# Kernel tuning notes

Hardware: AMD Instinct MI355X
Metric: run time of the kernel (lower is better)

Reference implementation:

```python
import jax, jax.numpy as jnp
import numpy as np

ALPHA = 0.2      # LeakyReLU slope
KNN_RANK = 6     # adj keeps ranks <= 6 (7 nearest incl. self)
NEG = -1e12


def _gat_layer(x, adj, W, a, concat):
    # x: [B,N,Cin], W: [Cin,Cout], a: [2*Cout,1]
    h = jnp.matmul(x, W)                      # [B,N,C]
    C = W.shape[1]
    f1 = jnp.matmul(h, a[:C, 0])              # [B,N]  a1^T h_i
    f2 = jnp.matmul(h, a[C:, 0])              # [B,N]  a2^T h_j
    e = jax.nn.leaky_relu(f1[:, :, None] + f2[:, None, :], ALPHA)  # [B,N,N]
    e = jnp.where(adj > 0, e, NEG)
    att = jax.nn.softmax(e, axis=2)
    hp = jnp.einsum('bij,bjc->bic', att, h)
    return jax.nn.relu(hp) if concat else hp


def _knn_adj(y):
    # y: [B,N,C]; euclidean cdist then rank-threshold (argsort.argsort <= 6)
    sq = jnp.sum(y * y, axis=-1)              # [B,N]
    d2 = sq[:, :, None] + sq[:, None, :] - 2.0 * jnp.einsum('bic,bjc->bij', y, y)
    dist = jnp.sqrt(jnp.clip(d2, 0.0))
    ranks = jnp.argsort(jnp.argsort(dist, axis=2), axis=2)
    return jax.lax.stop_gradient((ranks <= KNN_RANK).astype(y.dtype))


def reference(x, w_head, b_head, W0, a0, W1, a1, W_out, a_out, w_last, b_last):
    # head conv: k=3, stride=2, pad=1
    y = jax.lax.conv_general_dilated(
        x, w_head, window_strides=(2, 2), padding=((1, 1), (1, 1)),
        dimension_numbers=('NCHW', 'OIHW', 'NCHW')) + b_head[None, :, None, None]
    B, C, H, W = y.shape
    N = H * W
    yn = jnp.transpose(y.reshape(B, C, N), (0, 2, 1))   # [B,N,C]
    adj = _knn_adj(yn)

    # GAT: two concat heads, then out head, elu, log_softmax over channels
    h = jnp.concatenate([_gat_layer(yn, adj, W0, a0, True),
                         _gat_layer(yn, adj, W1, a1, True)], axis=2)
    out = jax.nn.elu(_gat_layer(h, adj, W_out, a_out, False))
    out = jax.nn.log_softmax(out, axis=2)               # [B,N,C]

    Ho = int(np.sqrt(N))
    z = jnp.transpose(out, (0, 2, 1)).reshape(B, C, Ho, Ho)
    # ConvTranspose2d(k=3, s=2, pad=1, output_pad=1) == dilated conv with
    # flipped, transposed kernel; padding low=k-1-p=1, high=k-1-p+op=2
    w_eq = jnp.flip(w_last, axis=(2, 3)).swapaxes(0, 1)  # (out,in,kh,kw)
    z = jax.lax.conv_general_dilated(
        z, w_eq, window_strides=(1, 1), padding=((1, 2), (1, 2)),
        lhs_dilation=(2, 2), dimension_numbers=('NCHW', 'OIHW', 'NCHW'))
    return z + b_last[None, :, None, None]


def setup_inputs() -> dict:
    key = jax.random.key(0)
    ks = jax.random.split(key, 12)
    Cin, Cout = 31, 64
    s = 0.05
    return {
        'x': jax.random.normal(ks[0], (2, Cin, 128, 128), jnp.float32),
        'w_head': jax.random.normal(ks[1], (Cout, Cin, 3, 3), jnp.float32) * s,
        'b_head': jnp.zeros((Cout,), jnp.float32),
        'W0': jax.random.normal(ks[2], (Cout, Cout), jnp.float32) * s,
        'a0': jax.random.normal(ks[3], (2 * Cout, 1), jnp.float32) * s,
        'W1': jax.random.normal(ks[4], (Cout, Cout), jnp.float32) * s,
        'a1': jax.random.normal(ks[5], (2 * Cout, 1), jnp.float32) * s,
        'W_out': jax.random.normal(ks[6], (2 * Cout, Cout), jnp.float32) * s,
        'a_out': jax.random.normal(ks[7], (2 * Cout, 1), jnp.float32) * s,
        'w_last': jax.random.normal(ks[8], (Cout, Cout, 3, 3), jnp.float32) * s,  # torch (in,out,kh,kw)
        'b_last': jnp.zeros((Cout,), jnp.float32),
    }
```

## Files before the change

### kernel.cpp

```cpp
#include <hip/hip_runtime.h>
#include <math.h>

#define B2     2
#define CIN    31
#define CC     64
#define NN     4096
#define NCH    8

typedef short bf16x8 __attribute__((ext_vector_type(8)));
typedef float f32x4  __attribute__((ext_vector_type(4)));

__device__ inline unsigned short f2bf(float f) {
  union { float f; unsigned u; } v; v.f = f;
  unsigned r = (v.u + 0x7fffu + ((v.u >> 16) & 1u)) >> 16;
  return (unsigned short)r;
}
__device__ inline float bf2f(unsigned short h) {
  union { float f; unsigned u; } v; v.u = ((unsigned)h) << 16;
  return v.f;
}

constexpr int OF_YN   = 0;
constexpr int OF_SQ   = OF_YN   + B2*NN*CC;
constexpr int OF_HCAT = OF_SQ   + B2*NN;
constexpr int OF_FV   = OF_HCAT + B2*NN*128;
constexpr int OF_HAGG = OF_FV   + 4*B2*NN;
constexpr int OF_HO   = OF_HAGG + B2*NN*128;
constexpr int OF_FO   = OF_HO   + B2*NN*CC;
constexpr int OF_Z    = OF_FO   + 2*B2*NN;
constexpr int OF_PD   = OF_Z    + B2*NN*CC;
constexpr int OF_PI   = OF_PD   + B2*NN*NCH*7;
constexpr int OF_NBR  = OF_PI   + B2*NN*NCH*7;
constexpr int OF_WT   = OF_NBR  + B2*NN*7;
constexpr int OF_WHT  = OF_WT   + 9*64*64;
constexpr int OF_YNH  = OF_WHT  + 279*64;
constexpr int OF_YNL  = OF_YNH  + B2*NN*CC/2;

__global__ __launch_bounds__(256) void k_prep(const float* __restrict__ wlast,
                                              const float* __restrict__ whead,
                                              float* __restrict__ wT,
                                              float* __restrict__ whT) {
  int idx = blockIdx.x*256 + threadIdx.x;
  if (idx < 36864) {
    int co = idx & 63, ci = (idx >> 6) & 63, kk = idx >> 12;
    wT[idx] = wlast[(ci*64 + co)*9 + kk];
  } else if (idx < 36864 + 279*64) {
    int j = idx - 36864;
    int c = j & 63, q = j >> 6;
    whT[j] = whead[c*279 + q];
  }
}

__global__ __launch_bounds__(256) void k_head(const float* __restrict__ x,
                                              const float* __restrict__ whT,
                                              const float* __restrict__ bias,
                                              float* __restrict__ yn,
                                              float* __restrict__ sq,
                                              unsigned short* __restrict__ ynh,
                                              unsigned short* __restrict__ ynl) {
  int lane = threadIdx.x & 63, wv = threadIdx.x >> 6;
  int gbase = blockIdx.x*8 + wv*2;
  __shared__ __align__(16) float patch[4][2][280];
  for (int nn = 0; nn < 2; ++nn) {
    int g = gbase + nn;
    int b = g >> 12, n = g & 4095;
    int oh = n >> 6, ow = n & 63;
    for (int q = lane; q < 279; q += 64) {
      int ci = q / 9, r = q - ci*9;
      int ky = r / 3, kx = r - ky*3;
      int ih = 2*oh - 1 + ky, iw = 2*ow - 1 + kx;
      float v = 0.f;
      if (ih >= 0 && ih < 128 && iw >= 0 && iw < 128)
        v = x[((b*CIN + ci)*128 + ih)*128 + iw];
      patch[wv][nn][q] = v;
    }
  }
  __syncthreads();
  int c = lane;
  float acc[2];
  float bv = bias[c];
  acc[0] = bv; acc[1] = bv;
  for (int q = 0; q < 276; q += 4) {
    float w0 = whT[q*64 + c];
    float w1 = whT[(q+1)*64 + c];
    float w2 = whT[(q+2)*64 + c];
    float w3 = whT[(q+3)*64 + c];
    #pragma unroll
    for (int nn = 0; nn < 2; ++nn) {
      float4 pv = *(const float4*)&patch[wv][nn][q];
      acc[nn] = fmaf(pv.x, w0, acc[nn]);
      acc[nn] = fmaf(pv.y, w1, acc[nn]);
      acc[nn] = fmaf(pv.z, w2, acc[nn]);
      acc[nn] = fmaf(pv.w, w3, acc[nn]);
    }
  }
  for (int q = 276; q < 279; ++q) {
    float wq = whT[q*64 + c];
    #pragma unroll
    for (int nn = 0; nn < 2; ++nn) acc[nn] = fmaf(patch[wv][nn][q], wq, acc[nn]);
  }
  for (int nn = 0; nn < 2; ++nn) {
    int g = gbase + nn;
    float y = acc[nn];
    yn[g*64 + c] = y;
    unsigned short hb = f2bf(y);
    ynh[g*64 + c] = hb;
    ynl[g*64 + c] = f2bf(y - bf2f(hb));
    float s = y*y;
    #pragma unroll
    for (int off = 32; off > 0; off >>= 1) s += __shfl_xor(s, off);
    if (lane == 0) sq[g] = s;
  }
}

__global__ __launch_bounds__(256, 4) void k_knn6(const unsigned short* __restrict__ ynh,
                                                 const unsigned short* __restrict__ ynl,
                                                 const float* __restrict__ sq,
                                                 float* __restrict__ pd,
                                                 int* __restrict__ pidx) {
  __shared__ __align__(16) unsigned short Bh[2][64*72];
  __shared__ __align__(16) unsigned short Bl[2][64*72];
  __shared__ __align__(16) float sqjs[2][64];

  int b = blockIdx.z, ib = blockIdx.x, jsp = blockIdx.y;
  int i0 = ib*64, jbase = jsp*512;
  int tid = threadIdx.x;
  int lane = tid & 63, w = tid >> 6;
  int quad = lane >> 4, m = lane & 15;

  const unsigned short* ynh_b = ynh + (size_t)b*NN*64;
  const unsigned short* ynl_b = ynl + (size_t)b*NN*64;
  const float* sq_b = sq + b*NN;

  int irow = i0 + w*16 + m;
  bf16x8 bhf0 = *(const bf16x8*)(ynh_b + irow*64 + quad*8);
  bf16x8 bhf1 = *(const bf16x8*)(ynh_b + irow*64 + 32 + quad*8);
  bf16x8 blf0 = *(const bf16x8*)(ynl_b + irow*64 + quad*8);
  bf16x8 blf1 = *(const bf16x8*)(ynl_b + irow*64 + 32 + quad*8);
  float sqi = sq_b[irow];

  unsigned k7[7];
  #pragma unroll
  for (int k = 0; k < 7; ++k) k7[k] = 0xFFFFFFFFu;

  int srow = tid >> 3, oct = tid & 7;

  {
    int jt = jbase;
    *(uint4*)&Bh[0][srow*72 + oct*8]      = *(const uint4*)(ynh_b + (jt + srow)*64 + oct*8);
    *(uint4*)&Bh[0][(srow+32)*72 + oct*8] = *(const uint4*)(ynh_b + (jt + srow + 32)*64 + oct*8);
    *(uint4*)&Bl[0][srow*72 + oct*8]      = *(const uint4*)(ynl_b + (jt + srow)*64 + oct*8);
    *(uint4*)&Bl[0][(srow+32)*72 + oct*8] = *(const uint4*)(ynl_b + (jt + srow + 32)*64 + oct*8);
    if (tid < 64) sqjs[0][tid] = sq_b[jt + tid];
  }
  __syncthreads();

  #pragma unroll 1
  for (int c = 0; c < 8; ++c) {
    int buf = c & 1, nbuf = buf ^ 1;
    uint4 gh0, gh1, gl0, gl1; float gsq = 0.f;
    if (c < 7) {
      int jt = jbase + (c+1)*64;
      gh0 = *(const uint4*)(ynh_b + (jt + srow)*64 + oct*8);
      gh1 = *(const uint4*)(ynh_b + (jt + srow + 32)*64 + oct*8);
      gl0 = *(const uint4*)(ynl_b + (jt + srow)*64 + oct*8);
      gl1 = *(const uint4*)(ynl_b + (jt + srow + 32)*64 + oct*8);
      if (tid < 64) gsq = sq_b[jt + tid];
    }
    unsigned lc = (unsigned)(c << 4);
    #pragma unroll
    for (int jn = 0; jn < 4; ++jn) {
      const int ro = (jn*16 + m)*72 + quad*8;
      bf16x8 ajh0 = *(const bf16x8*)&Bh[buf][ro];
      bf16x8 ajh1 = *(const bf16x8*)&Bh[buf][ro + 32];
      bf16x8 ajl0 = *(const bf16x8*)&Bl[buf][ro];
      bf16x8 ajl1 = *(const bf16x8*)&Bl[buf][ro + 32];
      f32x4 sq4 = *(const f32x4*)&sqjs[buf][jn*16 + quad*4];

      f32x4 a = (f32x4){0.f, 0.f, 0.f, 0.f};
      a = __builtin_amdgcn_mfma_f32_16x16x32_bf16(ajh0, bhf0, a, 0, 0, 0);
      a = __builtin_amdgcn_mfma_f32_16x16x32_bf16(ajl0, bhf0, a, 0, 0, 0);
      a = __builtin_amdgcn_mfma_f32_16x16x32_bf16(ajh0, blf0, a, 0, 0, 0);
      a = __builtin_amdgcn_mfma_f32_16x16x32_bf16(ajh1, bhf1, a, 0, 0, 0);
      a = __builtin_amdgcn_mfma_f32_16x16x32_bf16(ajl1, bhf1, a, 0, 0, 0);
      a = __builtin_amdgcn_mfma_f32_16x16x32_bf16(ajh1, blf1, a, 0, 0, 0);

      #pragma unroll
      for (int r = 0; r < 4; ++r) {
        float d2v = fmaf(-2.f, a[r], sqi + sq4[r]);
        d2v = fmaxf(d2v, 0.f);
        unsigned mx = (__float_as_uint(d2v) & 0xFFFFFF80u) | (lc + (unsigned)(jn*4 + r));
        #pragma unroll
        for (int t7 = 0; t7 < 7; ++t7) {
          unsigned old = k7[t7];
          k7[t7] = (mx < old) ? mx : old;
          mx     = (mx < old) ? old : mx;
        }
      }
    }
    if (c < 7) {
      *(uint4*)&Bh[nbuf][srow*72 + oct*8]      = gh0;
      *(uint4*)&Bh[nbuf][(srow+32)*72 + oct*8] = gh1;
      *(uint4*)&Bl[nbuf][srow*72 + oct*8]      = gl0;
      *(uint4*)&Bl[nbuf][(srow+32)*72 + oct*8] = gl1;
      if (tid < 64) sqjs[nbuf][tid] = gsq;
    }
    __syncthreads();
  }

  float* cd = (float*)&Bh[0][0];
  int*   ci = (int*)&Bh[1][0];
  int row = w*16 + m;
  #pragma unroll
  for (int k = 0; k < 7; ++k) {
    unsigned key = k7[k];
    int local = key & 127;
    int cch = local >> 4, jn2 = (local >> 2) & 3, r2 = local & 3;
    cd[row*28 + quad*7 + k] = __uint_as_float(key & 0xFFFFFF80u);
    ci[row*28 + quad*7 + k] = jbase + cch*64 + jn2*16 + quad*4 + r2;
  }
  __syncthreads();
  if (tid < 64) {
    float md[7]; int mi[7];
    #pragma unroll
    for (int k = 0; k < 7; ++k) { md[k] = 3.0e38f; mi[k] = 0x7fffffff; }
    for (int e = 0; e < 28; ++e) {
      float d = cd[tid*28 + e]; int jj = ci[tid*28 + e];
      if (d < md[6] || (d == md[6] && jj < mi[6])) {
        int k = 6;
        #pragma unroll
        for (int t = 5; t >= 0; --t)
          if (d < md[t] || (d == md[t] && jj < mi[t])) { md[t+1] = md[t]; mi[t+1] = mi[t]; k = t; }
        md[k] = d; mi[k] = jj;
      }
    }
    int g = b*NN + i0 + tid;
    int base = (g*NCH + jsp)*7;
    #pragma unroll
    for (int k = 0; k < 7; ++k) { pd[base+k] = md[k]; pidx[base+k] = mi[k]; }
  }
}

__global__ __launch_bounds__(256) void k_hm(const float* __restrict__ yn,
                                            const float* __restrict__ W0,
                                            const float* __restrict__ W1,
                                            const float* __restrict__ a0,
                                            const float* __restrict__ a1,
                                            float* __restrict__ hcat,
                                            float* __restrict__ fv,
                                            const float* __restrict__ pd,
                                            const int* __restrict__ pidx,
                                            int* __restrict__ nbr) {
  __shared__ __align__(16) float yt[16*64];
  int tid = threadIdx.x;
  if (blockIdx.x >= 512) {
    int g = (blockIdx.x - 512)*256 + tid;
    float d7[7]; int x7[7];
    #pragma unroll
    for (int k = 0; k < 7; ++k) { d7[k] = 3.0e38f; x7[k] = 0x7fffffff; }
    int base = g*NCH*7;
    for (int e = 0; e < NCH*7; ++e) {
      float d = pd[base+e]; int jj = pidx[base+e];
      if (d < d7[6]) {
        int k = 6;
        #pragma unroll
        for (int t = 5; t >= 0; --t) {
          if (d < d7[t]) { d7[t+1] = d7[t]; x7[t+1] = x7[t]; k = t; }
        }
        d7[k] = d; x7[k] = jj;
      }
    }
    #pragma unroll
    for (int k = 0; k < 7; ++k) nbr[g*7 + k] = x7[k];
    return;
  }
  int b = blockIdx.x >> 8, n0 = (blockIdx.x & 255)*16;
  int c = tid & 127, ng = tid >> 7, lane = tid & 63;
  float wreg[64];
  {
    const float* Wp = (c < 64) ? (W0 + c) : (W1 + (c - 64));
    #pragma unroll
    for (int k = 0; k < 64; ++k) wreg[k] = Wp[k*64];
  }
  ((float4*)yt)[tid] = ((const float4*)(yn + (b*NN + n0)*64))[tid];
  __syncthreads();
  int head = c >> 6;
  float av1 = head ? a1[lane] : a0[lane];
  float av2 = head ? a1[64 + lane] : a0[64 + lane];
  for (int nn = 0; nn < 8; ++nn) {
    int node = ng*8 + nn;
    const float* yr = yt + node*64;
    float acc = 0.f;
    #pragma unroll
    for (int k4 = 0; k4 < 16; ++k4) {
      float4 yv = *(const float4*)(yr + k4*4);
      acc = fmaf(yv.x, wreg[k4*4+0], acc);
      acc = fmaf(yv.y, wreg[k4*4+1], acc);
      acc = fmaf(yv.z, wreg[k4*4+2], acc);
      acc = fmaf(yv.w, wreg[k4*4+3], acc);
    }
    hcat[(b*NN + n0 + node)*128 + c] = acc;
    float s1 = acc*av1, s2 = acc*av2;
    #pragma unroll
    for (int off = 32; off > 0; off >>= 1) {
      s1 += __shfl_xor(s1, off); s2 += __shfl_xor(s2, off);
    }
    if (lane == 0) {
      int gg = (b << 12) + n0 + node;
      fv[head*16384 + gg] = s1;
      fv[head*16384 + 8192 + gg] = s2;
    }
  }
}

__global__ __launch_bounds__(256) void k_agg1(const float* __restrict__ hcat,
                                              const float* __restrict__ fv,
                                              const int* __restrict__ nbr,
                                              float* __restrict__ hagg) {
  int g = blockIdx.x*2 + (threadIdx.x >> 7);
  int c = threadIdx.x & 127;
  int b = g >> 12;
  int head = c >> 6;
  int jj[7];
  #pragma unroll
  for (int t = 0; t < 7; ++t) jj[t] = nbr[g*7 + t];
  float f1 = fv[head*16384 + g];
  const float* f2p = fv + head*16384 + 8192 + (b << 12);
  float e[7], mx = -3.0e38f;
  #pragma unroll
  for (int t = 0; t < 7; ++t) {
    float v = f1 + f2p[jj[t]];
    v = (v >= 0.f) ? v : 0.2f*v;
    e[t] = v; mx = fmaxf(mx, v);
  }
  float wgt[7], s = 0.f;
  #pragma unroll
  for (int t = 0; t < 7; ++t) { wgt[t] = expf(e[t] - mx); s += wgt[t]; }
  float acc = 0.f;
  #pragma unroll
  for (int t = 0; t < 7; ++t)
    acc += (wgt[t]/s) * hcat[((b << 12) + jj[t])*128 + c];
  hagg[g*128 + c] = fmaxf(acc, 0.f);
}

__global__ __launch_bounds__(256) void k_ho(const float* __restrict__ hagg,
                                            const float* __restrict__ Wout,
                                            const float* __restrict__ aout,
                                            float* __restrict__ ho,
                                            float* __restrict__ fo) {
  __shared__ __align__(16) float ht[16*128];
  __shared__ float part[16][64];
  int b = blockIdx.x >> 8, n0 = (blockIdx.x & 255)*16;
  int tid = threadIdx.x;
  int c = tid & 63, g = (tid >> 6) & 1, ng = tid >> 7;
  float wreg[64];
  #pragma unroll
  for (int k = 0; k < 64; ++k) wreg[k] = Wout[(g*64 + k)*64 + c];
  {
    const float4* src = (const float4*)(hagg + (b*NN + n0)*128);
    ((float4*)ht)[tid] = src[tid];
    ((float4*)ht)[tid + 256] = src[tid + 256];
  }
  __syncthreads();
  float accs[8];
  for (int nn = 0; nn < 8; ++nn) {
    int node = ng*8 + nn;
    const float* hr = ht + node*128 + g*64;
    float acc = 0.f;
    #pragma unroll
    for (int k4 = 0; k4 < 16; ++k4) {
      float4 hv = *(const float4*)(hr + k4*4);
      acc = fmaf(hv.x, wreg[k4*4+0], acc);
      acc = fmaf(hv.y, wreg[k4*4+1], acc);
      acc = fmaf(hv.z, wreg[k4*4+2], acc);
      acc = fmaf(hv.w, wreg[k4*4+3], acc);
    }
    accs[nn] = acc;
  }
  if (g == 0) {
    #pragma unroll
    for (int nn = 0; nn < 8; ++nn) part[ng*8 + nn][c] = accs[nn];
  }
  __syncthreads();
  if (g == 1) {
    float av1 = aout[c], av2 = aout[64 + c];
    for (int nn = 0; nn < 8; ++nn) {
      int node = ng*8 + nn;
      float acc = accs[nn] + part[node][c];
      ho[(b*NN + n0 + node)*64 + c] = acc;
      float s1 = acc*av1, s2 = acc*av2;
      #pragma unroll
      for (int off = 32; off > 0; off >>= 1) {
        s1 += __shfl_xor(s1, off); s2 += __shfl_xor(s2, off);
      }
      if (c == 0) {
        int gg = (b << 12) + n0 + node;
        fo[gg] = s1;
        fo[8192 + gg] = s2;
      }
    }
  }
}

__global__ __launch_bounds__(256) void k_agg2(const float* __restrict__ ho,
                                              const float* __restrict__ fo,
                                              const int* __restrict__ nbr,
                                              float* __restrict__ zbuf) {
  int g = blockIdx.x*4 + (threadIdx.x >> 6);
  int c = threadIdx.x & 63;
  int b = g >> 12;
  int jj[7];
  #pragma unroll
  for (int t = 0; t < 7; ++t) jj[t] = nbr[g*7 + t];
  float f1 = fo[g];
  const float* f2p = fo + 8192 + (b << 12);
  float e[7], mx = -3.0e38f;
  #pragma unroll
  for (int t = 0; t < 7; ++t) {
    float v = f1 + f2p[jj[t]];
    v = (v >= 0.f) ? v : 0.2f*v;
    e[t] = v; mx = fmaxf(mx, v);
  }
  float wgt[7], s = 0.f;
  #pragma unroll
  for (int t = 0; t < 7; ++t) { wgt[t] = expf(e[t] - mx); s += wgt[t]; }
  float acc = 0.f;
  #pragma unroll
  for (int t = 0; t < 7; ++t)
    acc += (wgt[t]/s) * ho[((b << 12) + jj[t])*64 + c];
  float v = (acc > 0.f) ? acc : expm1f(acc);
  float mm = v;
  #pragma unroll
  for (int off = 32; off > 0; off >>= 1) mm = fmaxf(mm, __shfl_xor(mm, off));
  float ex = expf(v - mm), ss = ex;
  #pragma unroll
  for (int off = 32; off > 0; off >>= 1) ss += __shfl_xor(ss, off);
  zbuf[g*64 + c] = v - mm - logf(ss);
}

__global__ __launch_bounds__(256, 4) void k_convt4(const float* __restrict__ z,
                                                   const float* __restrict__ wT,
                                                   const float* __restrict__ bias,
                                                   float* __restrict__ out) {
  __shared__ __align__(16) float lds[8704];
  float* zt = lds;
  float* ws = lds + 4608;
  float* so = lds;

  int oy = blockIdx.x, xh = blockIdx.y, b = blockIdx.z;
  int r = oy >> 1, pi = oy & 1;
  int tid = threadIdx.x;
  int colo = tid & 15, pgrp = tid >> 4;
  int co4 = colo*4, m0 = pgrp*2;
  int ix0 = xh*32;

  int nrows = pi ? 2 : 1;
  for (int row = 0; row < nrows; ++row) {
    int iy = r + row;
    const float* zsrc = z + (((b << 12) + iy*64) << 6);
    float4 v[3];
    #pragma unroll
    for (int j = 0; j < 3; ++j) {
      int chunk = tid + j*256;
      float4 vv = {0.f, 0.f, 0.f, 0.f};
      if (chunk < 528) {
        int ix = chunk >> 4, ci4 = (chunk & 15) << 2;
        int ixg = ix0 + ix;
        if (ixg < 64 && iy < 64) vv = *(const float4*)(zsrc + ixg*64 + ci4);
      }
      v[j] = vv;
    }
    #pragma unroll
    for (int j = 0; j < 3; ++j) {
      int chunk = tid + j*256;
      if (chunk < 528) {
        int ix = chunk >> 4, ci4 = (chunk & 15) << 2;
        zt[row*2304 + (ci4+0)*36 + ix] = v[j].x;
        zt[row*2304 + (ci4+1)*36 + ix] = v[j].y;
        zt[row*2304 + (ci4+2)*36 + ix] = v[j].z;
        zt[row*2304 + (ci4+3)*36 + ix] = v[j].w;
      }
    }
  }

  float acc[2][2][4];
  {
    float4 bv = *(const float4*)&bias[co4];
    #pragma unroll
    for (int chi = 0; chi < 2; ++chi)
      #pragma unroll
      for (int k = 0; k < 2; ++k) {
        acc[chi][k][0] = bv.x; acc[chi][k][1] = bv.y;
        acc[chi][k][2] = bv.z; acc[chi][k][3] = bv.w;
      }
  }

  int kys[2], rows[2], nky;
  if (pi == 0) { kys[0] = 1; rows[0] = 0; nky = 1; }
  else         { kys[0] = 2; rows[0] = 0; kys[1] = 0; rows[1] = 1; nky = 2; }

  for (int t = 0; t < nky; ++t) {
    const float* zrow = zt + rows[t]*2304;
    for (int kx = 0; kx < 3; ++kx) {
      const float* wsrc = wT + (kys[t]*3 + kx)*4096;
      __syncthreads();
      {
        float4 wv4[4];
        #pragma unroll
        for (int j = 0; j < 4; ++j)
          wv4[j] = *(const float4*)(wsrc + (tid + j*256)*4);
        #pragma unroll
        for (int j = 0; j < 4; ++j)
          *(float4*)&ws[(tid + j*256)*4] = wv4[j];
      }
      __syncthreads();
      const int chi = (kx == 1) ? 0 : 1;
      const int xoff = (kx == 0) ? 1 : 0;
      float* ap = &acc[chi][0][0];
      for (int ci = 0; ci < 64; ++ci) {
        float4 wv = *(const float4*)&ws[ci*64 + co4];
        const float* zp = zrow + ci*36 + m0;
        float z0, z1;
        if (xoff == 0) { float2 za = *(const float2*)zp; z0 = za.x; z1 = za.y; }
        else           { float2 za = *(const float2*)zp; z0 = za.y; z1 = zp[2]; }
        ap[0] = fmaf(z0, wv.x, ap[0]);
        ap[1] = fmaf(z0, wv.y, ap[1]);
        ap[2] = fmaf(z0, wv.z, ap[2]);
        ap[3] = fmaf(z0, wv.w, ap[3]);
        ap[4] = fmaf(z1, wv.x, ap[4]);
        ap[5] = fmaf(z1, wv.y, ap[5]);
        ap[6] = fmaf(z1, wv.z, ap[6]);
        ap[7] = fmaf(z1, wv.w, ap[7]);
      }
    }
  }

  __syncthreads();
  #pragma unroll
  for (int chi = 0; chi < 2; ++chi)
    #pragma unroll
    for (int k = 0; k < 2; ++k)
      #pragma unroll
      for (int cc = 0; cc < 4; ++cc)
        so[(co4 + cc)*65 + 2*(m0 + k) + chi] = acc[chi][k][cc];
  __syncthreads();
  for (int idx = tid; idx < 4096; idx += 256) {
    int co = idx >> 6, ox = idx & 63;
    out[(((b << 6) + co)*128 + oy)*128 + xh*64 + ox] = so[co*65 + ox];
  }
}

extern "C" void kernel_launch(void* const* d_in, const int* in_sizes, int n_in,
                              void* d_out, int out_size, void* d_ws, size_t ws_size,
                              hipStream_t stream) {
  const float* x      = (const float*)d_in[0];
  const float* w_head = (const float*)d_in[1];
  const float* b_head = (const float*)d_in[2];
  const float* W0     = (const float*)d_in[3];
  const float* a0     = (const float*)d_in[4];
  const float* W1     = (const float*)d_in[5];
  const float* a1     = (const float*)d_in[6];
  const float* W_out  = (const float*)d_in[7];
  const float* a_out  = (const float*)d_in[8];
  const float* w_last = (const float*)d_in[9];
  const float* b_last = (const float*)d_in[10];
  float* out = (float*)d_out;

  float* wsf = (float*)d_ws;
  int*   wsi = (int*)d_ws;
  float* yn   = wsf + OF_YN;
  float* sq   = wsf + OF_SQ;
  float* hcat = wsf + OF_HCAT;
  float* fv   = wsf + OF_FV;
  float* hagg = wsf + OF_HAGG;
  float* ho   = wsf + OF_HO;
  float* fo   = wsf + OF_FO;
  float* zbuf = wsf + OF_Z;
  float* pd   = wsf + OF_PD;
  int*   pidx = wsi + OF_PI;
  int*   nbr  = wsi + OF_NBR;
  float* wT   = wsf + OF_WT;
  float* whT  = wsf + OF_WHT;
  unsigned short* ynh = (unsigned short*)(wsf + OF_YNH);
  unsigned short* ynl = (unsigned short*)(wsf + OF_YNL);

  hipLaunchKernelGGL(k_prep,  dim3(214), dim3(256), 0, stream, w_last, w_head, wT, whT);
  hipLaunchKernelGGL(k_head,  dim3(1024), dim3(256), 0, stream, x, whT, b_head, yn, sq, ynh, ynl);
  hipLaunchKernelGGL(k_knn6,  dim3(64, NCH, 2), dim3(256), 0, stream, ynh, ynl, sq, pd, pidx);
  hipLaunchKernelGGL(k_hm,    dim3(544), dim3(256), 0, stream, yn, W0, W1, a0, a1, hcat, fv, pd, pidx, nbr);
  hipLaunchKernelGGL(k_agg1,  dim3(4096), dim3(256), 0, stream, hcat, fv, nbr, hagg);
  hipLaunchKernelGGL(k_ho,    dim3(512), dim3(256), 0, stream, hagg, W_out, a_out, ho, fo);
  hipLaunchKernelGGL(k_agg2,  dim3(2048), dim3(256), 0, stream, ho, fo, nbr, zbuf);
  hipLaunchKernelGGL(k_convt4, dim3(128, 2, 2), dim3(256), 0, stream, zbuf, wT, b_last, out);
}
```

Baseline: 196.0 us.

## Fuse first GAT aggregation into output projection; shrink kNN tile to 32 columns

Result: slower. 203.8 us (+4.0%).

```diff
diff --git a/kernel.cpp b/kernel.cpp
--- a/kernel.cpp
+++ b/kernel.cpp
@@ -113,14 +113,14 @@
   }
 }
 
-__global__ __launch_bounds__(256, 4) void k_knn6(const unsigned short* __restrict__ ynh,
+__global__ __launch_bounds__(256, 8) void k_knn7(const unsigned short* __restrict__ ynh,
                                                  const unsigned short* __restrict__ ynl,
                                                  const float* __restrict__ sq,
                                                  float* __restrict__ pd,
                                                  int* __restrict__ pidx) {
-  __shared__ __align__(16) unsigned short Bh[2][64*72];
-  __shared__ __align__(16) unsigned short Bl[2][64*72];
-  __shared__ __align__(16) float sqjs[2][64];
+  __shared__ __align__(16) unsigned short Bh[2][32*72];
+  __shared__ __align__(16) unsigned short Bl[2][32*72];
+  __shared__ __align__(16) float sqjs[2][32];
 
   int b = blockIdx.z, ib = blockIdx.x, jsp = blockIdx.y;
   int i0 = ib*64, jbase = jsp*512;
@@ -147,29 +147,25 @@
 
   {
     int jt = jbase;
-    *(uint4*)&Bh[0][srow*72 + oct*8]      = *(const uint4*)(ynh_b + (jt + srow)*64 + oct*8);
-    *(uint4*)&Bh[0][(srow+32)*72 + oct*8] = *(const uint4*)(ynh_b + (jt + srow + 32)*64 + oct*8);
-    *(uint4*)&Bl[0][srow*72 + oct*8]      = *(const uint4*)(ynl_b + (jt + srow)*64 + oct*8);
-    *(uint4*)&Bl[0][(srow+32)*72 + oct*8] = *(const uint4*)(ynl_b + (jt + srow + 32)*64 + oct*8);
-    if (tid < 64) sqjs[0][tid] = sq_b[jt + tid];
+    *(uint4*)&Bh[0][srow*72 + oct*8] = *(const uint4*)(ynh_b + (jt + srow)*64 + oct*8);
+    *(uint4*)&Bl[0][srow*72 + oct*8] = *(const uint4*)(ynl_b + (jt + srow)*64 + oct*8);
+    if (tid < 32) sqjs[0][tid] = sq_b[jt + tid];
   }
   __syncthreads();
 
   #pragma unroll 1
-  for (int c = 0; c < 8; ++c) {
+  for (int c = 0; c < 16; ++c) {
     int buf = c & 1, nbuf = buf ^ 1;
-    uint4 gh0, gh1, gl0, gl1; float gsq = 0.f;
-    if (c < 7) {
-      int jt = jbase + (c+1)*64;
-      gh0 = *(const uint4*)(ynh_b + (jt + srow)*64 + oct*8);
-      gh1 = *(const uint4*)(ynh_b + (jt + srow + 32)*64 + oct*8);
-      gl0 = *(const uint4*)(ynl_b + (jt + srow)*64 + oct*8);
-      gl1 = *(const uint4*)(ynl_b + (jt + srow + 32)*64 + oct*8);
-      if (tid < 64) gsq = sq_b[jt + tid];
-    }
-    unsigned lc = (unsigned)(c << 4);
-    #pragma unroll
-    for (int jn = 0; jn < 4; ++jn) {
+    uint4 gh, gl; float gsq = 0.f;
+    if (c < 15) {
+      int jt = jbase + (c+1)*32;
+      gh = *(const uint4*)(ynh_b + (jt + srow)*64 + oct*8);
+      gl = *(const uint4*)(ynl_b + (jt + srow)*64 + oct*8);
+      if (tid < 32) gsq = sq_b[jt + tid];
+    }
+    unsigned lc = (unsigned)(c << 3);
+    #pragma unroll
+    for (int jn = 0; jn < 2; ++jn) {
       const int ro = (jn*16 + m)*72 + quad*8;
       bf16x8 ajh0 = *(const bf16x8*)&Bh[buf][ro];
       bf16x8 ajh1 = *(const bf16x8*)&Bh[buf][ro + 32];
@@ -198,26 +194,25 @@
         }
       }
     }
-    if (c < 7) {
-      *(uint4*)&Bh[nbuf][srow*72 + oct*8]      = gh0;
-      *(uint4*)&Bh[nbuf][(srow+32)*72 + oct*8] = gh1;
-      *(uint4*)&Bl[nbuf][srow*72 + oct*8]      = gl0;
-      *(uint4*)&Bl[nbuf][(srow+32)*72 + oct*8] = gl1;
-      if (tid < 64) sqjs[nbuf][tid] = gsq;
+    if (c < 15) {
+      *(uint4*)&Bh[nbuf][srow*72 + oct*8] = gh;
+      *(uint4*)&Bl[nbuf][srow*72 + oct*8] = gl;
+      if (tid < 32) sqjs[nbuf][tid] = gsq;
     }
     __syncthreads();
   }
 
   float* cd = (float*)&Bh[0][0];
-  int*   ci = (int*)&Bh[1][0];
+  int*   ci = (int*)&Bl[0][0];
   int row = w*16 + m;
   #pragma unroll
   for (int k = 0; k < 7; ++k) {
     unsigned key = k7[k];
     int local = key & 127;
-    int cch = local >> 4, jn2 = (local >> 2) & 3, r2 = local & 3;
+    int cch = local >> 3, rem = local & 7;
+    int jn2 = rem >> 2, r2 = rem & 3;
     cd[row*28 + quad*7 + k] = __uint_as_float(key & 0xFFFFFF80u);
-    ci[row*28 + quad*7 + k] = jbase + cch*64 + jn2*16 + quad*4 + r2;
+    ci[row*28 + quad*7 + k] = jbase + cch*32 + jn2*16 + quad*4 + r2;
   }
   __syncthreads();
   if (tid < 64) {
@@ -313,55 +308,52 @@
   }
 }
 
-__global__ __launch_bounds__(256) void k_agg1(const float* __restrict__ hcat,
-                                              const float* __restrict__ fv,
-                                              const int* __restrict__ nbr,
-                                              float* __restrict__ hagg) {
-  int g = blockIdx.x*2 + (threadIdx.x >> 7);
-  int c = threadIdx.x & 127;
-  int b = g >> 12;
-  int head = c >> 6;
-  int jj[7];
-  #pragma unroll
-  for (int t = 0; t < 7; ++t) jj[t] = nbr[g*7 + t];
-  float f1 = fv[head*16384 + g];
-  const float* f2p = fv + head*16384 + 8192 + (b << 12);
-  float e[7], mx = -3.0e38f;
-  #pragma unroll
-  for (int t = 0; t < 7; ++t) {
-    float v = f1 + f2p[jj[t]];
-    v = (v >= 0.f) ? v : 0.2f*v;
-    e[t] = v; mx = fmaxf(mx, v);
-  }
-  float wgt[7], s = 0.f;
-  #pragma unroll
-  for (int t = 0; t < 7; ++t) { wgt[t] = expf(e[t] - mx); s += wgt[t]; }
-  float acc = 0.f;
-  #pragma unroll
-  for (int t = 0; t < 7; ++t)
-    acc += (wgt[t]/s) * hcat[((b << 12) + jj[t])*128 + c];
-  hagg[g*128 + c] = fmaxf(acc, 0.f);
-}
-
-__global__ __launch_bounds__(256) void k_ho(const float* __restrict__ hagg,
-                                            const float* __restrict__ Wout,
-                                            const float* __restrict__ aout,
-                                            float* __restrict__ ho,
-                                            float* __restrict__ fo) {
+__global__ __launch_bounds__(256) void k_aggho(const float* __restrict__ hcat,
+                                               const float* __restrict__ fv,
+                                               const int* __restrict__ nbr,
+                                               const float* __restrict__ Wout,
+                                               const float* __restrict__ aout,
+                                               float* __restrict__ ho,
+                                               float* __restrict__ fo) {
   __shared__ __align__(16) float ht[16*128];
   __shared__ float part[16][64];
   int b = blockIdx.x >> 8, n0 = (blockIdx.x & 255)*16;
   int tid = threadIdx.x;
+
+  {
+    int c = tid & 127, half = tid >> 7;
+    int head = c >> 6;
+    const float* f2p = fv + head*16384 + 8192 + (b << 12);
+    for (int nn = 0; nn < 8; ++nn) {
+      int node = half*8 + nn;
+      int g = (b << 12) + n0 + node;
+      int jj[7];
+      #pragma unroll
+      for (int t = 0; t < 7; ++t) jj[t] = nbr[g*7 + t];
+      float f1 = fv[head*16384 + g];
+      float e[7], mx = -3.0e38f;
+      #pragma unroll
+      for (int t = 0; t < 7; ++t) {
+        float v = f1 + f2p[jj[t]];
+        v = (v >= 0.f) ? v : 0.2f*v;
+        e[t] = v; mx = fmaxf(mx, v);
+      }
+      float wgt[7], s = 0.f;
+      #pragma unroll
+      for (int t = 0; t < 7; ++t) { wgt[t] = expf(e[t] - mx); s += wgt[t]; }
+      float acc = 0.f;
+      #pragma unroll
+      for (int t = 0; t < 7; ++t)
+        acc += (wgt[t]/s) * hcat[((b << 12) + jj[t])*128 + c];
+      ht[node*128 + c] = fmaxf(acc, 0.f);
+    }
+  }
+  __syncthreads();
+
   int c = tid & 63, g = (tid >> 6) & 1, ng = tid >> 7;
   float wreg[64];
   #pragma unroll
   for (int k = 0; k < 64; ++k) wreg[k] = Wout[(g*64 + k)*64 + c];
-  {
-    const float4* src = (const float4*)(hagg + (b*NN + n0)*128);
-    ((float4*)ht)[tid] = src[tid];
-    ((float4*)ht)[tid + 256] = src[tid + 256];
-  }
-  __syncthreads();
   float accs[8];
   for (int nn = 0; nn < 8; ++nn) {
     int node = ng*8 + nn;
@@ -572,7 +564,6 @@
   float* sq   = wsf + OF_SQ;
   float* hcat = wsf + OF_HCAT;
   float* fv   = wsf + OF_FV;
-  float* hagg = wsf + OF_HAGG;
   float* ho   = wsf + OF_HO;
   float* fo   = wsf + OF_FO;
   float* zbuf = wsf + OF_Z;
@@ -586,10 +577,9 @@
 
   hipLaunchKernelGGL(k_prep,  dim3(214), dim3(256), 0, stream, w_last, w_head, wT, whT);
   hipLaunchKernelGGL(k_head,  dim3(1024), dim3(256), 0, stream, x, whT, b_head, yn, sq, ynh, ynl);
-  hipLaunchKernelGGL(k_knn6,  dim3(64, NCH, 2), dim3(256), 0, stream, ynh, ynl, sq, pd, pidx);
+  hipLaunchKernelGGL(k_knn7,  dim3(64, NCH, 2), dim3(256), 0, stream, ynh, ynl, sq, pd, pidx);
   hipLaunchKernelGGL(k_hm,    dim3(544), dim3(256), 0, stream, yn, W0, W1, a0, a1, hcat, fv, pd, pidx, nbr);
-  hipLaunchKernelGGL(k_agg1,  dim3(4096), dim3(256), 0, stream, hcat, fv, nbr, hagg);
-  hipLaunchKernelGGL(k_ho,    dim3(512), dim3(256), 0, stream, hagg, W_out, a_out, ho, fo);
+  hipLaunchKernelGGL(k_aggho, dim3(512), dim3(256), 0, stream, hcat, fv, nbr, W_out, a_out, ho, fo);
   hipLaunchKernelGGL(k_agg2,  dim3(2048), dim3(256), 0, stream, ho, fo, nbr, zbuf);
   hipLaunchKernelGGL(k_convt4, dim3(128, 2, 2), dim3(256), 0, stream, zbuf, wT, b_last, out);
 }
```

## Fuse first GAT aggregation into output projection and shrink conv-transpose tiles

Applied to the files above, without the earlier changes.

After: 202.4 us. +3.3%, slower.

```diff
diff --git a/kernel.cpp b/kernel.cpp
--- a/kernel.cpp
+++ b/kernel.cpp
@@ -313,55 +313,52 @@
   }
 }
 
-__global__ __launch_bounds__(256) void k_agg1(const float* __restrict__ hcat,
-                                              const float* __restrict__ fv,
-                                              const int* __restrict__ nbr,
-                                              float* __restrict__ hagg) {
-  int g = blockIdx.x*2 + (threadIdx.x >> 7);
-  int c = threadIdx.x & 127;
-  int b = g >> 12;
-  int head = c >> 6;
-  int jj[7];
-  #pragma unroll
-  for (int t = 0; t < 7; ++t) jj[t] = nbr[g*7 + t];
-  float f1 = fv[head*16384 + g];
-  const float* f2p = fv + head*16384 + 8192 + (b << 12);
-  float e[7], mx = -3.0e38f;
-  #pragma unroll
-  for (int t = 0; t < 7; ++t) {
-    float v = f1 + f2p[jj[t]];
-    v = (v >= 0.f) ? v : 0.2f*v;
-    e[t] = v; mx = fmaxf(mx, v);
-  }
-  float wgt[7], s = 0.f;
-  #pragma unroll
-  for (int t = 0; t < 7; ++t) { wgt[t] = expf(e[t] - mx); s += wgt[t]; }
-  float acc = 0.f;
-  #pragma unroll
-  for (int t = 0; t < 7; ++t)
-    acc += (wgt[t]/s) * hcat[((b << 12) + jj[t])*128 + c];
-  hagg[g*128 + c] = fmaxf(acc, 0.f);
-}
-
-__global__ __launch_bounds__(256) void k_ho(const float* __restrict__ hagg,
-                                            const float* __restrict__ Wout,
-                                            const float* __restrict__ aout,
-                                            float* __restrict__ ho,
-                                            float* __restrict__ fo) {
+__global__ __launch_bounds__(256) void k_aggho(const float* __restrict__ hcat,
+                                               const float* __restrict__ fv,
+                                               const int* __restrict__ nbr,
+                                               const float* __restrict__ Wout,
+                                               const float* __restrict__ aout,
+                                               float* __restrict__ ho,
+                                               float* __restrict__ fo) {
   __shared__ __align__(16) float ht[16*128];
   __shared__ float part[16][64];
   int b = blockIdx.x >> 8, n0 = (blockIdx.x & 255)*16;
   int tid = threadIdx.x;
+
+  {
+    int c = tid & 127, half = tid >> 7;
+    int head = c >> 6;
+    const float* f2p = fv + head*16384 + 8192 + (b << 12);
+    for (int nn = 0; nn < 8; ++nn) {
+      int node = half*8 + nn;
+      int g = (b << 12) + n0 + node;
+      int jj[7];
+      #pragma unroll
+      for (int t = 0; t < 7; ++t) jj[t] = nbr[g*7 + t];
+      float f1 = fv[head*16384 + g];
+      float e[7], mx = -3.0e38f;
+      #pragma unroll
+      for (int t = 0; t < 7; ++t) {
+        float v = f1 + f2p[jj[t]];
+        v = (v >= 0.f) ? v : 0.2f*v;
+        e[t] = v; mx = fmaxf(mx, v);
+      }
+      float wgt[7], s = 0.f;
+      #pragma unroll
+      for (int t = 0; t < 7; ++t) { wgt[t] = expf(e[t] - mx); s += wgt[t]; }
+      float acc = 0.f;
+      #pragma unroll
+      for (int t = 0; t < 7; ++t)
+        acc += (wgt[t]/s) * hcat[((b << 12) + jj[t])*128 + c];
+      ht[node*128 + c] = fmaxf(acc, 0.f);
+    }
+  }
+  __syncthreads();
+
   int c = tid & 63, g = (tid >> 6) & 1, ng = tid >> 7;
   float wreg[64];
   #pragma unroll
   for (int k = 0; k < 64; ++k) wreg[k] = Wout[(g*64 + k)*64 + c];
-  {
-    const float4* src = (const float4*)(hagg + (b*NN + n0)*128);
-    ((float4*)ht)[tid] = src[tid];
-    ((float4*)ht)[tid + 256] = src[tid + 256];
-  }
-  __syncthreads();
   float accs[8];
   for (int nn = 0; nn < 8; ++nn) {
     int node = ng*8 + nn;
@@ -438,32 +435,32 @@
   zbuf[g*64 + c] = v - mm - logf(ss);
 }
 
-__global__ __launch_bounds__(256, 4) void k_convt4(const float* __restrict__ z,
+__global__ __launch_bounds__(256, 4) void k_convt6(const float* __restrict__ z,
                                                    const float* __restrict__ wT,
                                                    const float* __restrict__ bias,
                                                    float* __restrict__ out) {
-  __shared__ __align__(16) float lds[8704];
+  __shared__ __align__(16) float lds[6656];
   float* zt = lds;
-  float* ws = lds + 4608;
+  float* ws = lds + 2560;
   float* so = lds;
 
-  int oy = blockIdx.x, xh = blockIdx.y, b = blockIdx.z;
+  int oy = blockIdx.x, xq = blockIdx.y, b = blockIdx.z;
   int r = oy >> 1, pi = oy & 1;
   int tid = threadIdx.x;
   int colo = tid & 15, pgrp = tid >> 4;
-  int co4 = colo*4, m0 = pgrp*2;
-  int ix0 = xh*32;
+  int co4 = colo*4;
+  int ix0 = xq*16;
 
   int nrows = pi ? 2 : 1;
   for (int row = 0; row < nrows; ++row) {
     int iy = r + row;
     const float* zsrc = z + (((b << 12) + iy*64) << 6);
-    float4 v[3];
-    #pragma unroll
-    for (int j = 0; j < 3; ++j) {
+    float4 v[2];
+    #pragma unroll
+    for (int j = 0; j < 2; ++j) {
       int chunk = tid + j*256;
       float4 vv = {0.f, 0.f, 0.f, 0.f};
-      if (chunk < 528) {
+      if (chunk < 272) {
         int ix = chunk >> 4, ci4 = (chunk & 15) << 2;
         int ixg = ix0 + ix;
         if (ixg < 64 && iy < 64) vv = *(const float4*)(zsrc + ixg*64 + ci4);
@@ -471,28 +468,26 @@
       v[j] = vv;
     }
     #pragma unroll
-    for (int j = 0; j < 3; ++j) {
+    for (int j = 0; j < 2; ++j) {
       int chunk = tid + j*256;
-      if (chunk < 528) {
+      if (chunk < 272) {
         int ix = chunk >> 4, ci4 = (chunk & 15) << 2;
-        zt[row*2304 + (ci4+0)*36 + ix] = v[j].x;
-        zt[row*2304 + (ci4+1)*36 + ix] = v[j].y;
-        zt[row*2304 + (ci4+2)*36 + ix] = v[j].z;
-        zt[row*2304 + (ci4+3)*36 + ix] = v[j].w;
-      }
-    }
-  }
-
-  float acc[2][2][4];
+        zt[row*1280 + (ci4+0)*20 + ix] = v[j].x;
+        zt[row*1280 + (ci4+1)*20 + ix] = v[j].y;
+        zt[row*1280 + (ci4+2)*20 + ix] = v[j].z;
+        zt[row*1280 + (ci4+3)*20 + ix] = v[j].w;
+      }
+    }
+  }
+
+  float acc[2][4];
   {
     float4 bv = *(const float4*)&bias[co4];
     #pragma unroll
-    for (int chi = 0; chi < 2; ++chi)
-      #pragma unroll
-      for (int k = 0; k < 2; ++k) {
-        acc[chi][k][0] = bv.x; acc[chi][k][1] = bv.y;
-        acc[chi][k][2] = bv.z; acc[chi][k][3] = bv.w;
-      }
+    for (int chi = 0; chi < 2; ++chi) {
+      acc[chi][0] = bv.x; acc[chi][1] = bv.y;
+      acc[chi][2] = bv.z; acc[chi][3] = bv.w;
+    }
   }
 
   int kys[2], rows[2], nky;
@@ -500,7 +495,7 @@
   else         { kys[0] = 2; rows[0] = 0; kys[1] = 0; rows[1] = 1; nky = 2; }
 
   for (int t = 0; t < nky; ++t) {
-    const float* zrow = zt + rows[t]*2304;
+    const float* zrow = zt + rows[t]*1280;
     for (int kx = 0; kx < 3; ++kx) {
       const float* wsrc = wT + (kys[t]*3 + kx)*4096;
       __syncthreads();
@@ -515,22 +510,15 @@
       }
       __syncthreads();
       const int chi = (kx == 1) ? 0 : 1;
-      const int xoff = (kx == 0) ? 1 : 0;
-      float* ap = &acc[chi][0][0];
+      const int zi = pgrp + ((kx == 0) ? 1 : 0);
+      float* ap = acc[chi];
       for (int ci = 0; ci < 64; ++ci) {
         float4 wv = *(const float4*)&ws[ci*64 + co4];
-        const float* zp = zrow + ci*36 + m0;
-        float z0, z1;
-        if (xoff == 0) { float2 za = *(const float2*)zp; z0 = za.x; z1 = za.y; }
-        else           { float2 za = *(const float2*)zp; z0 = za.y; z1 = zp[2]; }
-        ap[0] = fmaf(z0, wv.x, ap[0]);
-        ap[1] = fmaf(z0, wv.y, ap[1]);
-        ap[2] = fmaf(z0, wv.z, ap[2]);
-        ap[3] = fmaf(z0, wv.w, ap[3]);
-        ap[4] = fmaf(z1, wv.x, ap[4]);
-        ap[5] = fmaf(z1, wv.y, ap[5]);
-        ap[6] = fmaf(z1, wv.z, ap[6]);
-        ap[7] = fmaf(z1, wv.w, ap[7]);
+        float zv = zrow[ci*20 + zi];
+        ap[0] = fmaf(zv, wv.x, ap[0]);
+        ap[1] = fmaf(zv, wv.y, ap[1]);
+        ap[2] = fmaf(zv, wv.z, ap[2]);
+        ap[3] = fmaf(zv, wv.w, ap[3]);
       }
     }
   }
@@ -539,14 +527,12 @@
   #pragma unroll
   for (int chi = 0; chi < 2; ++chi)
     #pragma unroll
-    for (int k = 0; k < 2; ++k)
-      #pragma unroll
-      for (int cc = 0; cc < 4; ++cc)
-        so[(co4 + cc)*65 + 2*(m0 + k) + chi] = acc[chi][k][cc];
-  __syncthreads();
-  for (int idx = tid; idx < 4096; idx += 256) {
-    int co = idx >> 6, ox = idx & 63;
-    out[(((b << 6) + co)*128 + oy)*128 + xh*64 + ox] = so[co*65 + ox];
+    for (int cc = 0; cc < 4; ++cc)
+      so[(co4 + cc)*33 + 2*pgrp + chi] = acc[chi][cc];
+  __syncthreads();
+  for (int idx = tid; idx < 2048; idx += 256) {
+    int co = idx >> 5, ox = idx & 31;
+    out[(((b << 6) + co)*128 + oy)*128 + xq*32 + ox] = so[co*33 + ox];
   }
 }
 
@@ -572,7 +558,6 @@
   float* sq   = wsf + OF_SQ;
   float* hcat = wsf + OF_HCAT;
   float* fv   = wsf + OF_FV;
-  float* hagg = wsf + OF_HAGG;
   float* ho   = wsf + OF_HO;
   float* fo   = wsf + OF_FO;
   float* zbuf = wsf + OF_Z;
@@ -588,8 +573,7 @@
   hipLaunchKernelGGL(k_head,  dim3(1024), dim3(256), 0, stream, x, whT, b_head, yn, sq, ynh, ynl);
   hipLaunchKernelGGL(k_knn6,  dim3(64, NCH, 2), dim3(256), 0, stream, ynh, ynl, sq, pd, pidx);
   hipLaunchKernelGGL(k_hm,    dim3(544), dim3(256), 0, stream, yn, W0, W1, a0, a1, hcat, fv, pd, pidx, nbr);
-  hipLaunchKernelGGL(k_agg1,  dim3(4096), dim3(256), 0, stream, hcat, fv, nbr, hagg);
-  hipLaunchKernelGGL(k_ho,    dim3(512), dim3(256), 0, stream, hagg, W_out, a_out, ho, fo);
+  hipLaunchKernelGGL(k_aggho, dim3(512), dim3(256), 0, stream, hcat, fv, nbr, W_out, a_out, ho, fo);
   hipLaunchKernelGGL(k_agg2,  dim3(2048), dim3(256), 0, stream, ho, fo, nbr, zbuf);
-  hipLaunchKernelGGL(k_convt4, dim3(128, 2, 2), dim3(256), 0, stream, zbuf, wT, b_last, out);
-}
+  hipLaunchKernelGGL(k_convt6, dim3(128, 4, 2), dim3(256), 0, stream, zbuf, wT, b_last, out);
+}
```
